# Performance work log

Measured on AMD Instinct MI355X. Metric: run time of the kernel, lower is better.

## Reference

```python
import jax, jax.numpy as jnp
import numpy as np

H, D, DIM = 8, 128, 1024   # heads, dim_head, model dim (inner_dim = H*D = DIM)
QB, N = 16, 512            # 'q' and 'n' dims of the [q, n, dim] inputs


def layer_norm(x, g, b, eps=1e-5):
    mu = x.mean(-1, keepdims=True)
    var = ((x - mu) ** 2).mean(-1, keepdims=True)
    return (x - mu) / jnp.sqrt(var + eps) * g + b


def setup_inputs() -> dict:
    key = jax.random.key(0)
    ks = jax.random.split(key, 8)
    rn = lambda k, shape, s=1.0: jax.random.normal(k, shape, jnp.float32) * s
    return {
        'q': rn(ks[0], (QB, N, DIM)),
        'k': rn(ks[1], (QB, N, DIM)),
        'v': rn(ks[2], (QB, N, DIM)),
        'ln_g': jnp.ones(DIM, jnp.float32),
        'ln_b': jnp.zeros(DIM, jnp.float32),
        'w_in': rn(ks[3], (H * D, DIM), 0.02),          # Linear(dim -> inner_dim), no bias
        'wp_w1': rn(ks[4], (D, 2 * D), 0.05),           # weight_predictor Linear(2d -> d)
        'wp_b1': jnp.zeros(D, jnp.float32),
        'wp_ln_g': jnp.ones(D, jnp.float32),
        'wp_ln_b': jnp.zeros(D, jnp.float32),
        'wp_w2': rn(ks[5], (3, D), 0.05),               # Linear(d -> 3)
        'wp_b2': jnp.zeros(3, jnp.float32),
        'w_out': rn(ks[6], (DIM, H * D), 0.02),         # output Linear(inner_dim -> dim)
        'b_out': jnp.zeros(DIM, jnp.float32),
    }


def reference(q, k, v, ln_g, ln_b, w_in, wp_w1, wp_b1, wp_ln_g, wp_ln_b,
              wp_w2, wp_b2, w_out, b_out):
    def proj(t):
        x = layer_norm(t, ln_g, ln_b) @ w_in.T                 # [Q, N, H*D]
        Qd, Nd = t.shape[0], t.shape[1]
        return x.reshape(Qd, Nd, H, D).transpose(2, 0, 1, 3)   # [h, q, n, d]

    f_q, f_k, f_v = proj(q), proj(k), proj(v)

    # cosine similarity component
    dots = jnp.einsum('hqnd,hqmd->hqnm', f_q, f_k)
    qn = jnp.linalg.norm(f_q, axis=-1)                          # [h, q, n]
    kn = jnp.linalg.norm(f_k, axis=-1)                          # [h, q, m]
    cosine_sim = dots / (qn[..., :, None] * kn[..., None, :])

    q_centered = f_q - f_q.mean(-1, keepdims=True)

    # variance component (unbiased variance, clipped ratio vs target_var=1)
    q_var = jnp.var(f_q, axis=-1, ddof=1)
    k_var = jnp.var(f_k, axis=-1, ddof=1)
    q_ratio = 2.0 * jnp.minimum(q_var, 1.0) / (q_var + 1.0)
    k_ratio = 2.0 * jnp.minimum(k_var, 1.0) / (k_var + 1.0)
    var_component = jnp.einsum('hqn,hqm->hqnm', q_ratio, k_ratio)

    # decorrelation-scaled covariance component (overwrites the dead loop in the source)
    q_flat = q_centered.reshape(H, -1, D)                        # [h, q*n, d]
    feat_corr = jnp.einsum('hnd,hne->hde', q_flat, q_flat) / q_flat.shape[1]
    feat_corr = feat_corr * (1.0 - jnp.eye(D, dtype=feat_corr.dtype))
    decorr_score = jnp.linalg.norm(feat_corr, axis=(-2, -1)) / (D * D)
    decorr_scale = jnp.exp(-5.0 * decorr_score)[:, None, None, None]
    cov_component = cosine_sim * decorr_scale

    # dynamic per-head weight mixing
    q_global = f_q.mean(axis=(1, 2))                             # [h, d]
    k_global = f_k.mean(axis=(1, 2))
    feats = jnp.concatenate([q_global, k_global], axis=-1)       # [h, 2d]
    h1 = jnp.maximum(layer_norm(feats @ wp_w1.T + wp_b1, wp_ln_g, wp_ln_b), 0.0)
    weights = jax.nn.softmax(h1 @ wp_w2.T + wp_b2, axis=-1)      # [h, 3]
    cw = weights[:, 0][:, None, None, None]
    vw = weights[:, 1][:, None, None, None]
    ww = weights[:, 2][:, None, None, None]
    mixed = cw * cosine_sim + vw * cov_component + ww * var_component

    out = jnp.einsum('hqnm,hqmd->hqnd', mixed, f_v)
    out = out.transpose(1, 2, 0, 3).reshape(q.shape[0], q.shape[1], H * D)
    return out @ w_out.T + b_out
```

## Files before the change

### kernel.cpp

```cpp
#include <hip/hip_runtime.h>
#include <hip/hip_bf16.h>

typedef unsigned short u16;
typedef __attribute__((ext_vector_type(8))) short short8;
typedef __attribute__((ext_vector_type(4))) float floatx4;

#define H 8
#define D 128
#define DIM 1024
#define QB 16
#define NSEQ 512
#define R 8192

__device__ inline u16 f2b(float x) {
    union { float f; unsigned int u; } c{x};
    unsigned int lsb = (c.u >> 16) & 1;
    unsigned int r = c.u + 0x7fffu + lsb;
    return (u16)(r >> 16);
}
__device__ inline float b2f(u16 u) {
    union { unsigned int i; float f; } c;
    c.i = (unsigned int)u << 16;
    return c.f;
}

#define GLOAD_LDS16(gptr, lptr)                                                        \
    __builtin_amdgcn_global_load_lds(                                                  \
        (const __attribute__((address_space(1))) unsigned int*)(gptr),                 \
        (__attribute__((address_space(3))) unsigned int*)(lptr), 16, 0, 0)

__global__ __launch_bounds__(256) void ln_all(const float* __restrict__ q,
                                              const float* __restrict__ k,
                                              const float* __restrict__ v,
                                              const float* __restrict__ g,
                                              const float* __restrict__ b,
                                              u16* __restrict__ out) {
    const float* src = (blockIdx.y == 0) ? q : (blockIdx.y == 1) ? k : v;
    int r = blockIdx.x;
    int tid = threadIdx.x;
    const float* row = src + (size_t)r * DIM;
    float4 vv = *(const float4*)(row + tid * 4);
    float sum = vv.x + vv.y + vv.z + vv.w;
    float sq = vv.x * vv.x + vv.y * vv.y + vv.z * vv.z + vv.w * vv.w;
    __shared__ float s1[256], s2[256];
    s1[tid] = sum; s2[tid] = sq;
    __syncthreads();
    for (int s = 128; s > 0; s >>= 1) {
        if (tid < s) { s1[tid] += s1[tid + s]; s2[tid] += s2[tid + s]; }
        __syncthreads();
    }
    float mean = s1[0] * (1.0f / DIM);
    float var = s2[0] * (1.0f / DIM) - mean * mean;
    float rstd = rsqrtf(var + 1e-5f);
    float4 gv = *(const float4*)(g + tid * 4);
    float4 bv = *(const float4*)(b + tid * 4);
    ushort4 pk;
    pk.x = f2b((vv.x - mean) * rstd * gv.x + bv.x);
    pk.y = f2b((vv.y - mean) * rstd * gv.y + bv.y);
    pk.z = f2b((vv.z - mean) * rstd * gv.z + bv.z);
    pk.w = f2b((vv.w - mean) * rstd * gv.w + bv.w);
    *(ushort4*)(out + ((size_t)blockIdx.y * R + r) * DIM + tid * 4) = pk;
}

__global__ __launch_bounds__(256) void cvt2_kernel(const float* __restrict__ a,
                                                   const float* __restrict__ b,
                                                   u16* __restrict__ oa,
                                                   u16* __restrict__ ob, int n4each) {
    int i = blockIdx.x * 256 + threadIdx.x;
    const float* src; u16* dst; int j;
    if (i < n4each) { src = a; dst = oa; j = i; }
    else            { src = b; dst = ob; j = i - n4each; }
    float4 v = *(const float4*)(src + (size_t)j * 4);
    ushort4 pk;
    pk.x = f2b(v.x); pk.y = f2b(v.y); pk.z = f2b(v.z); pk.w = f2b(v.w);
    *(ushort4*)(dst + (size_t)j * 4) = pk;
}

__global__ __launch_bounds__(256) void gemm_qkv(const u16* __restrict__ A,
                                                const u16* __restrict__ B,
                                                u16* __restrict__ qT,
                                                u16* __restrict__ fqb,
                                                u16* __restrict__ kTh,
                                                u16* __restrict__ vT,
                                                float* __restrict__ qn,
                                                float* __restrict__ qm,
                                                float* __restrict__ qr,
                                                float* __restrict__ kn,
                                                float* __restrict__ kr) {
    __shared__ u16 As[128 * 32];
    __shared__ u16 Bs[128 * 32];
    const int tid = threadIdx.x;
    const int m0 = blockIdx.y * 128, n0 = blockIdx.x * 128;
    const int wave = tid >> 6, lane = tid & 63;
    const int wm = (wave >> 1) * 64, wn = (wave & 1) * 64;
    const int fr = lane & 15, kq = lane >> 4;
    const int srow = tid >> 2, scol = (tid & 3) * 8;

    floatx4 acc[4][4] = {};
    const size_t aOff0 = (size_t)(m0 + srow) * DIM + scol;
    const size_t aOff1 = (size_t)(m0 + 64 + srow) * DIM + scol;
    const size_t bOff0 = (size_t)(n0 + srow) * DIM + scol;
    const size_t bOff1 = (size_t)(n0 + 64 + srow) * DIM + scol;

    for (int kt = 0; kt < DIM; kt += 32) {
        GLOAD_LDS16(A + aOff0 + kt, As + tid * 8);
        GLOAD_LDS16(A + aOff1 + kt, As + (256 + tid) * 8);
        GLOAD_LDS16(B + bOff0 + kt, Bs + tid * 8);
        GLOAD_LDS16(B + bOff1 + kt, Bs + (256 + tid) * 8);
        __syncthreads();
        short8 af[4], bf[4];
#pragma unroll
        for (int i = 0; i < 4; i++)
            af[i] = *(const short8*)&As[(wm + i * 16 + fr) * 32 + kq * 8];
#pragma unroll
        for (int j = 0; j < 4; j++)
            bf[j] = *(const short8*)&Bs[(wn + j * 16 + fr) * 32 + kq * 8];
#pragma unroll
        for (int i = 0; i < 4; i++)
#pragma unroll
            for (int j = 0; j < 4; j++)
                acc[i][j] = __builtin_amdgcn_mfma_f32_16x16x32_bf16(af[i], bf[j], acc[i][j], 0, 0, 0);
        __syncthreads();
    }

    const int seg = blockIdx.y >> 6;
    const int lrb = (blockIdx.y & 63) * 128;
    const int h = blockIdx.x;
    float* sred = (float*)As;
    float* invb = (float*)Bs;

    if (seg <= 1) {
        const int half = wn >> 6;
#pragma unroll
        for (int i = 0; i < 4; i++) {
            float s[4] = {}, qs[4] = {};
#pragma unroll
            for (int j = 0; j < 4; j++)
#pragma unroll
                for (int r = 0; r < 4; r++) {
                    float vv = acc[i][j][r];
                    s[r] += vv; qs[r] += vv * vv;
                }
#pragma unroll
            for (int m = 1; m < 16; m <<= 1)
#pragma unroll
                for (int r = 0; r < 4; r++) {
                    s[r] += __shfl_xor(s[r], m);
                    qs[r] += __shfl_xor(qs[r], m);
                }
            if (fr == 0) {
                int row = wm + i * 16 + kq * 4;
#pragma unroll
                for (int r = 0; r < 4; r++) {
                    sred[(row + r) * 4 + half * 2 + 0] = s[r];
                    sred[(row + r) * 4 + half * 2 + 1] = qs[r];
                }
            }
        }
        __syncthreads();
        if (tid < 128) {
            float sum = sred[tid * 4 + 0] + sred[tid * 4 + 2];
            float sq  = sred[tid * 4 + 1] + sred[tid * 4 + 3];
            float nrm = sqrtf(sq);
            float var = (sq - sum * sum * (1.0f / D)) * (1.0f / (D - 1));
            float ratio = 2.0f * fminf(var, 1.0f) / (var + 1.0f);
            size_t idx = (size_t)h * R + lrb + tid;
            if (seg == 0) {
                qn[idx] = nrm; qm[idx] = sum * (1.0f / D); qr[idx] = ratio;
            } else {
                kn[idx] = nrm; kr[idx] = ratio;
                invb[tid] = 1.0f / nrm;
            }
        }
        __syncthreads();
    }

    u16* dstT = (seg == 0) ? qT : (seg == 1) ? kTh : vT;
#pragma unroll
    for (int i = 0; i < 4; i++) {
        const int tr = wm + i * 16 + kq * 4;
        const int lrow = lrb + tr;
        float sc[4] = {1.0f, 1.0f, 1.0f, 1.0f};
        if (seg == 1) {
#pragma unroll
            for (int r = 0; r < 4; r++) sc[r] = invb[tr + r];
        }
#pragma unroll
        for (int j = 0; j < 4; j++) {
            const int cl = wn + j * 16 + fr;
            ushort4 pk;
            pk.x = f2b(acc[i][j][0] * sc[0]);
            pk.y = f2b(acc[i][j][1] * sc[1]);
            pk.z = f2b(acc[i][j][2] * sc[2]);
            pk.w = f2b(acc[i][j][3] * sc[3]);
            *(ushort4*)(dstT + (size_t)(h * D + cl) * R + lrow) = pk;
            if (seg == 0) {
                fqb[(size_t)(lrow + 0) * DIM + h * D + cl] = pk.x;
                fqb[(size_t)(lrow + 1) * DIM + h * D + cl] = pk.y;
                fqb[(size_t)(lrow + 2) * DIM + h * D + cl] = pk.z;
                fqb[(size_t)(lrow + 3) * DIM + h * D + cl] = pk.w;
            }
        }
    }
}

template <int MODE>
__global__ __launch_bounds__(256) void colsum_b(const u16* __restrict__ fT,
                                                const float* __restrict__ wvec,
                                                float* __restrict__ g,
                                                float* __restrict__ u,
                                                float* __restrict__ s2) {
    int dg = blockIdx.x, h = blockIdx.y, tid = threadIdx.x;
    __shared__ float r1[256], r2[256];
    for (int dd = 0; dd < 8; dd++) {
        int d = dg * 8 + dd;
        const u16* rowp = fT + (size_t)(h * D + d) * R;
        float s = 0.0f, su = 0.0f;
        for (int it = 0; it < 32; it++) {
            int r = it * 256 + tid;
            float v = b2f(rowp[r]);
            if (MODE == 2) s += v * wvec[h * R + r];
            else { s += v; su += v * wvec[h * R + r]; }
        }
        r1[tid] = s; r2[tid] = su;
        __syncthreads();
        for (int st = 128; st > 0; st >>= 1) {
            if (tid < st) { r1[tid] += r1[tid + st]; r2[tid] += r2[tid + st]; }
            __syncthreads();
        }
        if (tid == 0) {
            g[h * D + d] = r1[0] * (1.0f / R);
            if (MODE == 1) u[h * D + d] = r2[0];
        }
        __syncthreads();
    }
    if (MODE == 1 && dg == 0) {
        float t = 0.0f;
        for (int it = 0; it < 32; it++) {
            float m = wvec[h * R + it * 256 + tid];
            t += m * m;
        }
        r1[tid] = t;
        __syncthreads();
        for (int st = 128; st > 0; st >>= 1) {
            if (tid < st) r1[tid] += r1[tid + st];
            __syncthreads();
        }
        if (tid == 0) s2[h] = r1[0];
    }
}

__global__ __launch_bounds__(256) void syrk_q(const u16* __restrict__ qT,
                                              float* __restrict__ P) {
    __shared__ u16 As[128 * 32];
    const int c = blockIdx.x, h = blockIdx.y;
    const int tid = threadIdx.x;
    const int wave = tid >> 6, lane = tid & 63;
    const int wm = (wave >> 1) * 64, wn = (wave & 1) * 64;
    const int fr = lane & 15, kq = lane >> 4;
    const int srow = tid >> 2, scol = (tid & 3) * 8;
    floatx4 acc[4][4] = {};
    const size_t a0 = (size_t)(h * D + srow) * R + c * 512 + scol;
    const size_t a1 = (size_t)(h * D + 64 + srow) * R + c * 512 + scol;
    for (int kt = 0; kt < 512; kt += 32) {
        GLOAD_LDS16(qT + a0 + kt, As + tid * 8);
        GLOAD_LDS16(qT + a1 + kt, As + (256 + tid) * 8);
        __syncthreads();
        short8 af[4], bf[4];
#pragma unroll
        for (int i = 0; i < 4; i++)
            af[i] = *(const short8*)&As[(wm + i * 16 + fr) * 32 + kq * 8];
#pragma unroll
        for (int j = 0; j < 4; j++)
            bf[j] = *(const short8*)&As[(wn + j * 16 + fr) * 32 + kq * 8];
#pragma unroll
        for (int i = 0; i < 4; i++)
#pragma unroll
            for (int j = 0; j < 4; j++)
                acc[i][j] = __builtin_amdgcn_mfma_f32_16x16x32_bf16(af[i], bf[j], acc[i][j], 0, 0, 0);
        __syncthreads();
    }
    float* base = P + (size_t)(h * 16 + c) * (D * D);
#pragma unroll
    for (int i = 0; i < 4; i++) {
        int dr = wm + i * 16 + kq * 4;
#pragma unroll
        for (int j = 0; j < 4; j++) {
            int ec = wn + j * 16 + fr;
#pragma unroll
            for (int r = 0; r < 4; r++)
                base[(size_t)(dr + r) * D + ec] = acc[i][j][r];
        }
    }
}

__global__ __launch_bounds__(256) void reduce_fc(const float* __restrict__ P,
                                                 float* __restrict__ fc) {
    int idx = blockIdx.x * 256 + threadIdx.x;
    int h = idx >> 14, de = idx & 16383;
    float s = 0.0f;
    for (int c = 0; c < 16; c++)
        s += P[(size_t)(h * 16 + c) * (D * D) + de];
    fc[idx] = s;
}

__global__ __launch_bounds__(256) void head_kernel(const float* __restrict__ fc,
                                                   const float* __restrict__ ubuf,
                                                   const float* __restrict__ s2b,
                                                   const float* __restrict__ qg,
                                                   const float* __restrict__ kg,
                                                   const float* __restrict__ w1,
                                                   const float* __restrict__ b1,
                                                   const float* __restrict__ lng,
                                                   const float* __restrict__ lnb,
                                                   const float* __restrict__ w2,
                                                   const float* __restrict__ b2,
                                                   float* __restrict__ coef) {
    int h = blockIdx.x, tid = threadIdx.x;
    __shared__ float s1[256], s2[256], s3[256];
    __shared__ float feats[256];
    float s2h = s2b[h];
    float S = 0.0f;
    for (int idx = tid; idx < D * D; idx += 256) {
        int dd = idx >> 7, ee = idx & 127;
        if (dd != ee) {
            float vv = (fc[h * (D * D) + idx] - ubuf[h * D + dd] - ubuf[h * D + ee] + s2h) * (1.0f / R);
            S += vv * vv;
        }
    }
    s1[tid] = S;
    __syncthreads();
    for (int s = 128; s > 0; s >>= 1) {
        if (tid < s) s1[tid] += s1[tid + s];
        __syncthreads();
    }
    float dscale = expf(-5.0f * sqrtf(s1[0]) / (float)(D * D));
    __syncthreads();
    feats[tid] = (tid < 128) ? qg[h * D + tid] : kg[h * D + tid - 128];
    __syncthreads();
    float yv = 0.0f;
    if (tid < 128) {
        float a = b1[tid];
        for (int i = 0; i < 256; i++) a = fmaf(feats[i], w1[tid * 256 + i], a);
        yv = a;
    }
    s1[tid] = (tid < 128) ? yv : 0.0f;
    s2[tid] = (tid < 128) ? yv * yv : 0.0f;
    __syncthreads();
    for (int s = 128; s > 0; s >>= 1) {
        if (tid < s) { s1[tid] += s1[tid + s]; s2[tid] += s2[tid + s]; }
        __syncthreads();
    }
    float mean = s1[0] * (1.0f / 128.0f);
    float var = s2[0] * (1.0f / 128.0f) - mean * mean;
    float rstd = rsqrtf(var + 1e-5f);
    float rel = 0.0f;
    if (tid < 128)
        rel = fmaxf((yv - mean) * rstd * lng[tid] + lnb[tid], 0.0f);
    __syncthreads();
    s1[tid] = (tid < 128) ? rel * w2[0 * 128 + tid] : 0.0f;
    s2[tid] = (tid < 128) ? rel * w2[1 * 128 + tid] : 0.0f;
    s3[tid] = (tid < 128) ? rel * w2[2 * 128 + tid] : 0.0f;
    __syncthreads();
    for (int s = 128; s > 0; s >>= 1) {
        if (tid < s) { s1[tid] += s1[tid + s]; s2[tid] += s2[tid + s]; s3[tid] += s3[tid + s]; }
        __syncthreads();
    }
    if (tid == 0) {
        float g0 = s1[0] + b2[0], g1 = s2[0] + b2[1], g2 = s3[0] + b2[2];
        float mx = fmaxf(g0, fmaxf(g1, g2));
        float e0 = expf(g0 - mx), e1 = expf(g1 - mx), e2 = expf(g2 - mx);
        float inv = 1.0f / (e0 + e1 + e2);
        coef[h * 2 + 0] = e0 * inv + e1 * inv * dscale;
        coef[h * 2 + 1] = e2 * inv;
    }
}

__global__ __launch_bounds__(256) void ktv_mfma(const u16* __restrict__ kTh,
                                                const u16* __restrict__ vT,
                                                const float* __restrict__ kr,
                                                u16* __restrict__ Mt,
                                                float* __restrict__ sv) {
    __shared__ u16 As[128 * 32];
    __shared__ u16 Bs[128 * 32];
    __shared__ float wbuf[32];
    __shared__ float svred[256];
    const int qi = blockIdx.x, h = blockIdx.y;
    const int tid = threadIdx.x;
    const int wave = tid >> 6, lane = tid & 63;
    const int wm = (wave >> 1) * 64, wn = (wave & 1) * 64;
    const int fr = lane & 15, kq = lane >> 4;
    const int srow = tid >> 2, scol = (tid & 3) * 8;
    const int m0g = qi * 512;
    const size_t a0 = (size_t)(h * D + srow) * R + m0g + scol;
    const size_t a1 = (size_t)(h * D + 64 + srow) * R + m0g + scol;
    const int e_id = tid & 127, eh = tid >> 7;
    float svacc = 0.0f;
    floatx4 acc[4][4] = {};
    for (int kt = 0; kt < 512; kt += 32) {
        GLOAD_LDS16(vT + a0 + kt, As + tid * 8);
        GLOAD_LDS16(vT + a1 + kt, As + (256 + tid) * 8);
        GLOAD_LDS16(kTh + a0 + kt, Bs + tid * 8);
        GLOAD_LDS16(kTh + a1 + kt, Bs + (256 + tid) * 8);
        if (tid < 32) wbuf[tid] = kr[(size_t)h * R + m0g + kt + tid];
        __syncthreads();
        short8 af[4], bf[4];
#pragma unroll
        for (int i = 0; i < 4; i++)
            af[i] = *(const short8*)&As[(wm + i * 16 + fr) * 32 + kq * 8];
#pragma unroll
        for (int j = 0; j < 4; j++)
            bf[j] = *(const short8*)&Bs[(wn + j * 16 + fr) * 32 + kq * 8];
#pragma unroll
        for (int i = 0; i < 4; i++)
#pragma unroll
            for (int j = 0; j < 4; j++)
                acc[i][j] = __builtin_amdgcn_mfma_f32_16x16x32_bf16(af[i], bf[j], acc[i][j], 0, 0, 0);
#pragma unroll
        for (int jm = 0; jm < 16; jm++) {
            int mm = eh * 16 + jm;
            svacc += b2f(As[e_id * 32 + mm]) * wbuf[mm];
        }
        __syncthreads();
    }
    u16* mb = Mt + (size_t)(h * QB + qi) * D * D;
#pragma unroll
    for (int i = 0; i < 4; i++) {
        int er = wm + i * 16 + kq * 4;
#pragma unroll
        for (int j = 0; j < 4; j++) {
            int dc = wn + j * 16 + fr;
#pragma unroll
            for (int r = 0; r < 4; r++)
                mb[(size_t)(er + r) * D + dc] = f2b(acc[i][j][r]);
        }
    }
    svred[tid] = svacc;
    __syncthreads();
    if (tid < 128)
        sv[(size_t)(h * QB + qi) * D + tid] = svred[tid] + svred[tid + 128];
}

__global__ __launch_bounds__(256) void attn_mfma(const u16* __restrict__ fqb,
                                                 const u16* __restrict__ Mt,
                                                 const float* __restrict__ qn,
                                                 const float* __restrict__ qr,
                                                 const float* __restrict__ sv,
                                                 const float* __restrict__ coef,
                                                 u16* __restrict__ outb) {
    __shared__ u16 As[128 * 32];
    __shared__ u16 Bs[128 * 32];
    const int nb = blockIdx.x, qi = blockIdx.y, h = blockIdx.z;
    const int tid = threadIdx.x;
    const int wave = tid >> 6, lane = tid & 63;
    const int wm = (wave >> 1) * 64, wn = (wave & 1) * 64;
    const int fr = lane & 15, kq = lane >> 4;
    const int srow = tid >> 2, scol = (tid & 3) * 8;
    const int n0g = qi * 512 + nb * 128;
    const size_t a0 = (size_t)(n0g + srow) * DIM + h * D + scol;
    const size_t a1 = (size_t)(n0g + 64 + srow) * DIM + h * D + scol;
    const u16* mtb = Mt + (size_t)(h * QB + qi) * D * D;
    floatx4 acc[4][4] = {};
    for (int kt = 0; kt < 128; kt += 32) {
        GLOAD_LDS16(fqb + a0 + kt, As + tid * 8);
        GLOAD_LDS16(fqb + a1 + kt, As + (256 + tid) * 8);
        GLOAD_LDS16(mtb + (size_t)srow * D + kt + scol, Bs + tid * 8);
        GLOAD_LDS16(mtb + (size_t)(64 + srow) * D + kt + scol, Bs + (256 + tid) * 8);
        __syncthreads();
        short8 af[4], bf[4];
#pragma unroll
        for (int i = 0; i < 4; i++)
            af[i] = *(const short8*)&As[(wm + i * 16 + fr) * 32 + kq * 8];
#pragma unroll
        for (int j = 0; j < 4; j++)
            bf[j] = *(const short8*)&Bs[(wn + j * 16 + fr) * 32 + kq * 8];
#pragma unroll
        for (int i = 0; i < 4; i++)
#pragma unroll
            for (int j = 0; j < 4; j++)
                acc[i][j] = __builtin_amdgcn_mfma_f32_16x16x32_bf16(af[i], bf[j], acc[i][j], 0, 0, 0);
        __syncthreads();
    }
    float c0 = coef[2 * h], c1 = coef[2 * h + 1];
#pragma unroll
    for (int i = 0; i < 4; i++) {
        int nr = n0g + wm + i * 16 + kq * 4;
        float sc1[4], sc2[4];
#pragma unroll
        for (int r = 0; r < 4; r++) {
            sc1[r] = c0 / qn[(size_t)h * R + nr + r];
            sc2[r] = c1 * qr[(size_t)h * R + nr + r];
        }
#pragma unroll
        for (int j = 0; j < 4; j++) {
            int ec = wn + j * 16 + fr;
            float svv = sv[(size_t)(h * QB + qi) * D + ec];
#pragma unroll
            for (int r = 0; r < 4; r++)
                outb[(size_t)(nr + r) * DIM + h * D + ec] = f2b(sc1[r] * acc[i][j][r] + sc2[r] * svv);
        }
    }
}

__global__ __launch_bounds__(256) void gemm_out(const u16* __restrict__ A,
                                                const u16* __restrict__ B,
                                                const float* __restrict__ bias,
                                                float* __restrict__ C) {
    __shared__ u16 As[128 * 32];
    __shared__ u16 Bs[128 * 32];
    const int tid = threadIdx.x;
    const int m0 = blockIdx.y * 128, n0 = blockIdx.x * 128;
    const int wave = tid >> 6, lane = tid & 63;
    const int wm = (wave >> 1) * 64, wn = (wave & 1) * 64;
    const int fr = lane & 15, kq = lane >> 4;
    const int srow = tid >> 2, scol = (tid & 3) * 8;
    floatx4 acc[4][4] = {};
    const size_t aOff0 = (size_t)(m0 + srow) * DIM + scol;
    const size_t aOff1 = (size_t)(m0 + 64 + srow) * DIM + scol;
    const size_t bOff0 = (size_t)(n0 + srow) * DIM + scol;
    const size_t bOff1 = (size_t)(n0 + 64 + srow) * DIM + scol;
    for (int kt = 0; kt < DIM; kt += 32) {
        GLOAD_LDS16(A + aOff0 + kt, As + tid * 8);
        GLOAD_LDS16(A + aOff1 + kt, As + (256 + tid) * 8);
        GLOAD_LDS16(B + bOff0 + kt, Bs + tid * 8);
        GLOAD_LDS16(B + bOff1 + kt, Bs + (256 + tid) * 8);
        __syncthreads();
        short8 af[4], bf[4];
#pragma unroll
        for (int i = 0; i < 4; i++)
            af[i] = *(const short8*)&As[(wm + i * 16 + fr) * 32 + kq * 8];
#pragma unroll
        for (int j = 0; j < 4; j++)
            bf[j] = *(const short8*)&Bs[(wn + j * 16 + fr) * 32 + kq * 8];
#pragma unroll
        for (int i = 0; i < 4; i++)
#pragma unroll
            for (int j = 0; j < 4; j++)
                acc[i][j] = __builtin_amdgcn_mfma_f32_16x16x32_bf16(af[i], bf[j], acc[i][j], 0, 0, 0);
        __syncthreads();
    }
#pragma unroll
    for (int i = 0; i < 4; i++) {
        int rbase = m0 + wm + i * 16 + kq * 4;
#pragma unroll
        for (int j = 0; j < 4; j++) {
            int col = n0 + wn + j * 16 + fr;
            float badd = bias[col];
#pragma unroll
            for (int r = 0; r < 4; r++)
                C[(size_t)(rbase + r) * DIM + col] = acc[i][j][r] + badd;
        }
    }
}

extern "C" void kernel_launch(void* const* d_in, const int* in_sizes, int n_in,
                              void* d_out, int out_size, void* d_ws, size_t ws_size,
                              hipStream_t stream) {
    (void)in_sizes; (void)n_in; (void)out_size; (void)ws_size;
    const float* q      = (const float*)d_in[0];
    const float* k      = (const float*)d_in[1];
    const float* v      = (const float*)d_in[2];
    const float* ln_g   = (const float*)d_in[3];
    const float* ln_b   = (const float*)d_in[4];
    const float* w_in   = (const float*)d_in[5];
    const float* wp_w1  = (const float*)d_in[6];
    const float* wp_b1  = (const float*)d_in[7];
    const float* wp_lng = (const float*)d_in[8];
    const float* wp_lnb = (const float*)d_in[9];
    const float* wp_w2  = (const float*)d_in[10];
    const float* wp_b2  = (const float*)d_in[11];
    const float* w_out  = (const float*)d_in[12];
    const float* b_out  = (const float*)d_in[13];
    float* out = (float*)d_out;

    constexpr size_t F = (size_t)R * DIM;
    u16* lnall   = (u16*)d_ws;
    u16* fqb     = lnall + 3 * F;
    u16* qT      = fqb + F;
    u16* kTh     = qT + F;
    u16* vT      = kTh + F;
    u16* w_in16  = vT + F;
    u16* w_out16 = w_in16 + (size_t)DIM * DIM;
    u16* Mt      = w_out16 + (size_t)DIM * DIM;
    float* P     = (float*)(Mt + (size_t)H * QB * D * D);
    float* fc    = P + (size_t)16 * H * D * D;
    float* qn    = fc + (size_t)H * D * D;
    float* qm    = qn + (size_t)H * R;
    float* qr    = qm + (size_t)H * R;
    float* kn    = qr + (size_t)H * R;
    float* kr    = kn + (size_t)H * R;
    float* qg    = kr + (size_t)H * R;
    float* kg    = qg + H * D;
    float* ubuf  = kg + H * D;
    float* s2    = ubuf + H * D;
    float* coef  = s2 + H;
    float* svb   = coef + 16;

    cvt2_kernel<<<2048, 256, 0, stream>>>(w_in, w_out, w_in16, w_out16, DIM * DIM / 4);
    ln_all<<<dim3(R, 3), 256, 0, stream>>>(q, k, v, ln_g, ln_b, lnall);

    gemm_qkv<<<dim3(DIM / 128, 3 * R / 128), 256, 0, stream>>>(
        lnall, w_in16, qT, fqb, kTh, vT, qn, qm, qr, kn, kr);

    colsum_b<1><<<dim3(16, H), 256, 0, stream>>>(qT, qm, qg, ubuf, s2);
    colsum_b<2><<<dim3(16, H), 256, 0, stream>>>(kTh, kn, kg, nullptr, nullptr);

    syrk_q<<<dim3(16, H), 256, 0, stream>>>(qT, P);
    reduce_fc<<<512, 256, 0, stream>>>(P, fc);

    head_kernel<<<H, 256, 0, stream>>>(fc, ubuf, s2, qg, kg, wp_w1, wp_b1,
                                       wp_lng, wp_lnb, wp_w2, wp_b2, coef);

    ktv_mfma<<<dim3(QB, H), 256, 0, stream>>>(kTh, vT, kr, Mt, svb);

    attn_mfma<<<dim3(4, QB, H), 256, 0, stream>>>(fqb, Mt, qn, qr, svb, coef, lnall);

    gemm_out<<<dim3(DIM / 128, R / 128), 256, 0, stream>>>(lnall, w_out16, b_out, out);
}
```

Measured before the change: 391.6 us.

## Transpose QKV MFMA operands, coalesce epilogue stores, remap blocks per XCD, fuse reductions

The QKV GEMM swaps MFMA operand order so each lane holds a row's values, which simplifies the row-stat reduction and the transposed stores. The fqb row-major copy is now staged through LDS and written as coalesced vectors. Both GEMMs use a 1D grid remapped so that consecutive row blocks land on the same XCD for L2 reuse. The two colsum launches merge into one, syrk splits K into 32 chunks, and reduce_fc plus the decorrelation sum fold into a parallel decorr_sum kernel in place of the single-block loop. In exchange, the transposed stores are now scalar 16-bit writes, and the larger LDS footprint may lower occupancy.

```diff
diff --git a/kernel.cpp b/kernel.cpp
--- a/kernel.cpp
+++ b/kernel.cpp
@@ -87,10 +87,21 @@
                                                 float* __restrict__ qr,
                                                 float* __restrict__ kn,
                                                 float* __restrict__ kr) {
-    __shared__ u16 As[128 * 32];
-    __shared__ u16 Bs[128 * 32];
+    __shared__ u16 smem[19712];
+    u16* As = smem;
+    u16* Bs = smem + 4096;
+    float* sred = (float*)(smem + 18432);
+    float* invb = (float*)(smem + 19456);
+
     const int tid = threadIdx.x;
-    const int m0 = blockIdx.y * 128, n0 = blockIdx.x * 128;
+    const int bb = blockIdx.x;
+    const int xcd = bb & 7, j0 = bb >> 3;
+    const int h = j0 & 7;
+    const int rowblk = xcd * 24 + (j0 >> 3);
+    const int m0 = rowblk * 128, n0 = h * 128;
+    const int seg = rowblk >> 6;
+    const int lrb = (rowblk & 63) * 128;
+
     const int wave = tid >> 6, lane = tid & 63;
     const int wm = (wave >> 1) * 64, wn = (wave & 1) * 64;
     const int fr = lane & 15, kq = lane >> 4;
@@ -108,53 +119,39 @@
         GLOAD_LDS16(B + bOff0 + kt, Bs + tid * 8);
         GLOAD_LDS16(B + bOff1 + kt, Bs + (256 + tid) * 8);
         __syncthreads();
-        short8 af[4], bf[4];
-#pragma unroll
-        for (int i = 0; i < 4; i++)
-            af[i] = *(const short8*)&As[(wm + i * 16 + fr) * 32 + kq * 8];
+        short8 xf[4], wf[4];
+#pragma unroll
+        for (int i = 0; i < 4; i++)
+            xf[i] = *(const short8*)&As[(wm + i * 16 + fr) * 32 + kq * 8];
 #pragma unroll
         for (int j = 0; j < 4; j++)
-            bf[j] = *(const short8*)&Bs[(wn + j * 16 + fr) * 32 + kq * 8];
-#pragma unroll
-        for (int i = 0; i < 4; i++)
-#pragma unroll
-            for (int j = 0; j < 4; j++)
-                acc[i][j] = __builtin_amdgcn_mfma_f32_16x16x32_bf16(af[i], bf[j], acc[i][j], 0, 0, 0);
-        __syncthreads();
-    }
-
-    const int seg = blockIdx.y >> 6;
-    const int lrb = (blockIdx.y & 63) * 128;
-    const int h = blockIdx.x;
-    float* sred = (float*)As;
-    float* invb = (float*)Bs;
+            wf[j] = *(const short8*)&Bs[(wn + j * 16 + fr) * 32 + kq * 8];
+#pragma unroll
+        for (int j = 0; j < 4; j++)
+#pragma unroll
+            for (int i = 0; i < 4; i++)
+                acc[j][i] = __builtin_amdgcn_mfma_f32_16x16x32_bf16(wf[j], xf[i], acc[j][i], 0, 0, 0);
+        __syncthreads();
+    }
 
     if (seg <= 1) {
         const int half = wn >> 6;
 #pragma unroll
         for (int i = 0; i < 4; i++) {
-            float s[4] = {}, qs[4] = {};
+            float s = 0.0f, qs = 0.0f;
 #pragma unroll
             for (int j = 0; j < 4; j++)
 #pragma unroll
-                for (int r = 0; r < 4; r++) {
-                    float vv = acc[i][j][r];
-                    s[r] += vv; qs[r] += vv * vv;
+                for (int rg = 0; rg < 4; rg++) {
+                    float vv = acc[j][i][rg];
+                    s += vv; qs += vv * vv;
                 }
-#pragma unroll
-            for (int m = 1; m < 16; m <<= 1)
-#pragma unroll
-                for (int r = 0; r < 4; r++) {
-                    s[r] += __shfl_xor(s[r], m);
-                    qs[r] += __shfl_xor(qs[r], m);
-                }
-            if (fr == 0) {
-                int row = wm + i * 16 + kq * 4;
-#pragma unroll
-                for (int r = 0; r < 4; r++) {
-                    sred[(row + r) * 4 + half * 2 + 0] = s[r];
-                    sred[(row + r) * 4 + half * 2 + 1] = qs[r];
-                }
+            s += __shfl_xor(s, 16); qs += __shfl_xor(qs, 16);
+            s += __shfl_xor(s, 32); qs += __shfl_xor(qs, 32);
+            if (kq == 0) {
+                int rl = wm + i * 16 + fr;
+                sred[rl * 4 + half * 2 + 0] = s;
+                sred[rl * 4 + half * 2 + 1] = qs;
             }
         }
         __syncthreads();
@@ -178,39 +175,52 @@
     u16* dstT = (seg == 0) ? qT : (seg == 1) ? kTh : vT;
 #pragma unroll
     for (int i = 0; i < 4; i++) {
-        const int tr = wm + i * 16 + kq * 4;
-        const int lrow = lrb + tr;
-        float sc[4] = {1.0f, 1.0f, 1.0f, 1.0f};
-        if (seg == 1) {
-#pragma unroll
-            for (int r = 0; r < 4; r++) sc[r] = invb[tr + r];
-        }
+        const int rl = wm + i * 16 + fr;
+        const float sc = (seg == 1) ? invb[rl] : 1.0f;
 #pragma unroll
         for (int j = 0; j < 4; j++) {
-            const int cl = wn + j * 16 + fr;
-            ushort4 pk;
-            pk.x = f2b(acc[i][j][0] * sc[0]);
-            pk.y = f2b(acc[i][j][1] * sc[1]);
-            pk.z = f2b(acc[i][j][2] * sc[2]);
-            pk.w = f2b(acc[i][j][3] * sc[3]);
-            *(ushort4*)(dstT + (size_t)(h * D + cl) * R + lrow) = pk;
-            if (seg == 0) {
-                fqb[(size_t)(lrow + 0) * DIM + h * D + cl] = pk.x;
-                fqb[(size_t)(lrow + 1) * DIM + h * D + cl] = pk.y;
-                fqb[(size_t)(lrow + 2) * DIM + h * D + cl] = pk.z;
-                fqb[(size_t)(lrow + 3) * DIM + h * D + cl] = pk.w;
+#pragma unroll
+            for (int rg = 0; rg < 4; rg++) {
+                const int cl = wn + j * 16 + kq * 4 + rg;
+                dstT[(size_t)(h * D + cl) * R + lrb + rl] = f2b(acc[j][i][rg] * sc);
             }
         }
     }
-}
-
-template <int MODE>
-__global__ __launch_bounds__(256) void colsum_b(const u16* __restrict__ fT,
-                                                const float* __restrict__ wvec,
-                                                float* __restrict__ g,
-                                                float* __restrict__ u,
-                                                float* __restrict__ s2) {
-    int dg = blockIdx.x, h = blockIdx.y, tid = threadIdx.x;
+
+    if (seg == 0) {
+        __syncthreads();
+        u16* Tw = smem + wave * 4608;
+#pragma unroll
+        for (int i = 0; i < 4; i++)
+#pragma unroll
+            for (int j = 0; j < 4; j++) {
+                ushort4 pk;
+                pk.x = f2b(acc[j][i][0]); pk.y = f2b(acc[j][i][1]);
+                pk.z = f2b(acc[j][i][2]); pk.w = f2b(acc[j][i][3]);
+                *(ushort4*)&Tw[(i * 16 + fr) * 72 + j * 16 + kq * 4] = pk;
+            }
+        __syncthreads();
+#pragma unroll
+        for (int p = 0; p < 16; p++) {
+            int rloc = p * 4 + kq;
+            int c4 = fr * 4;
+            ushort4 v = *(const ushort4*)&Tw[rloc * 72 + c4];
+            *(ushort4*)&fqb[(size_t)(lrb + wm + rloc) * DIM + h * D + wn + c4] = v;
+        }
+    }
+}
+
+__global__ __launch_bounds__(256) void colsum2(const u16* __restrict__ qT,
+                                               const u16* __restrict__ kTh,
+                                               const float* __restrict__ qm,
+                                               const float* __restrict__ kn,
+                                               float* __restrict__ qg,
+                                               float* __restrict__ kg,
+                                               float* __restrict__ ubuf,
+                                               float* __restrict__ s2) {
+    int dg = blockIdx.x, h = blockIdx.y, mode = blockIdx.z, tid = threadIdx.x;
+    const u16* fT = mode ? kTh : qT;
+    const float* wvec = mode ? kn : qm;
     __shared__ float r1[256], r2[256];
     for (int dd = 0; dd < 8; dd++) {
         int d = dg * 8 + dd;
@@ -219,8 +229,9 @@
         for (int it = 0; it < 32; it++) {
             int r = it * 256 + tid;
             float v = b2f(rowp[r]);
-            if (MODE == 2) s += v * wvec[h * R + r];
-            else { s += v; su += v * wvec[h * R + r]; }
+            float w = wvec[h * R + r];
+            if (mode) s += v * w;
+            else { s += v; su += v * w; }
         }
         r1[tid] = s; r2[tid] = su;
         __syncthreads();
@@ -229,15 +240,15 @@
             __syncthreads();
         }
         if (tid == 0) {
-            g[h * D + d] = r1[0] * (1.0f / R);
-            if (MODE == 1) u[h * D + d] = r2[0];
-        }
-        __syncthreads();
-    }
-    if (MODE == 1 && dg == 0) {
+            if (mode) kg[h * D + d] = r1[0] * (1.0f / R);
+            else { qg[h * D + d] = r1[0] * (1.0f / R); ubuf[h * D + d] = r2[0]; }
+        }
+        __syncthreads();
+    }
+    if (!mode && dg == 0) {
         float t = 0.0f;
         for (int it = 0; it < 32; it++) {
-            float m = wvec[h * R + it * 256 + tid];
+            float m = qm[h * R + it * 256 + tid];
             t += m * m;
         }
         r1[tid] = t;
@@ -260,9 +271,9 @@
     const int fr = lane & 15, kq = lane >> 4;
     const int srow = tid >> 2, scol = (tid & 3) * 8;
     floatx4 acc[4][4] = {};
-    const size_t a0 = (size_t)(h * D + srow) * R + c * 512 + scol;
-    const size_t a1 = (size_t)(h * D + 64 + srow) * R + c * 512 + scol;
-    for (int kt = 0; kt < 512; kt += 32) {
+    const size_t a0 = (size_t)(h * D + srow) * R + c * 256 + scol;
+    const size_t a1 = (size_t)(h * D + 64 + srow) * R + c * 256 + scol;
+    for (int kt = 0; kt < 256; kt += 32) {
         GLOAD_LDS16(qT + a0 + kt, As + tid * 8);
         GLOAD_LDS16(qT + a1 + kt, As + (256 + tid) * 8);
         __syncthreads();
@@ -280,7 +291,7 @@
                 acc[i][j] = __builtin_amdgcn_mfma_f32_16x16x32_bf16(af[i], bf[j], acc[i][j], 0, 0, 0);
         __syncthreads();
     }
-    float* base = P + (size_t)(h * 16 + c) * (D * D);
+    float* base = P + (size_t)(h * 32 + c) * (D * D);
 #pragma unroll
     for (int i = 0; i < 4; i++) {
         int dr = wm + i * 16 + kq * 4;
@@ -294,19 +305,35 @@
     }
 }
 
-__global__ __launch_bounds__(256) void reduce_fc(const float* __restrict__ P,
-                                                 float* __restrict__ fc) {
-    int idx = blockIdx.x * 256 + threadIdx.x;
-    int h = idx >> 14, de = idx & 16383;
-    float s = 0.0f;
-    for (int c = 0; c < 16; c++)
-        s += P[(size_t)(h * 16 + c) * (D * D) + de];
-    fc[idx] = s;
-}
-
-__global__ __launch_bounds__(256) void head_kernel(const float* __restrict__ fc,
-                                                   const float* __restrict__ ubuf,
-                                                   const float* __restrict__ s2b,
+__global__ __launch_bounds__(256) void decorr_sum(const float* __restrict__ P,
+                                                  const float* __restrict__ ubuf,
+                                                  const float* __restrict__ s2b,
+                                                  float* __restrict__ Spart) {
+    int bx = blockIdx.x, h = blockIdx.y, tid = threadIdx.x;
+    float s2h = s2b[h];
+    float S = 0.0f;
+    for (int t = 0; t < 8; t++) {
+        int de = bx * 2048 + t * 256 + tid;
+        int dd = de >> 7, ee = de & 127;
+        float g = 0.0f;
+        for (int c = 0; c < 32; c++)
+            g += P[(size_t)(h * 32 + c) * (D * D) + de];
+        if (dd != ee) {
+            float vv = (g - ubuf[h * D + dd] - ubuf[h * D + ee] + s2h) * (1.0f / R);
+            S += vv * vv;
+        }
+    }
+    __shared__ float r1[256];
+    r1[tid] = S;
+    __syncthreads();
+    for (int st = 128; st > 0; st >>= 1) {
+        if (tid < st) r1[tid] += r1[tid + st];
+        __syncthreads();
+    }
+    if (tid == 0) Spart[h * 8 + bx] = r1[0];
+}
+
+__global__ __launch_bounds__(256) void head_kernel(const float* __restrict__ Spart,
                                                    const float* __restrict__ qg,
                                                    const float* __restrict__ kg,
                                                    const float* __restrict__ w1,
@@ -319,23 +346,9 @@
     int h = blockIdx.x, tid = threadIdx.x;
     __shared__ float s1[256], s2[256], s3[256];
     __shared__ float feats[256];
-    float s2h = s2b[h];
-    float S = 0.0f;
-    for (int idx = tid; idx < D * D; idx += 256) {
-        int dd = idx >> 7, ee = idx & 127;
-        if (dd != ee) {
-            float vv = (fc[h * (D * D) + idx] - ubuf[h * D + dd] - ubuf[h * D + ee] + s2h) * (1.0f / R);
-            S += vv * vv;
-        }
-    }
-    s1[tid] = S;
-    __syncthreads();
-    for (int s = 128; s > 0; s >>= 1) {
-        if (tid < s) s1[tid] += s1[tid + s];
-        __syncthreads();
-    }
-    float dscale = expf(-5.0f * sqrtf(s1[0]) / (float)(D * D));
-    __syncthreads();
+    float Ssum = 0.0f;
+    for (int c = 0; c < 8; c++) Ssum += Spart[h * 8 + c];
+    float dscale = expf(-5.0f * sqrtf(Ssum) / (float)(D * D));
     feats[tid] = (tid < 128) ? qg[h * D + tid] : kg[h * D + tid - 128];
     __syncthreads();
     float yv = 0.0f;
@@ -509,7 +522,10 @@
     __shared__ u16 As[128 * 32];
     __shared__ u16 Bs[128 * 32];
     const int tid = threadIdx.x;
-    const int m0 = blockIdx.y * 128, n0 = blockIdx.x * 128;
+    const int bb = blockIdx.x;
+    const int xcd = bb & 7, jj = bb >> 3;
+    const int col = jj & 7, rowblk = xcd * 8 + (jj >> 3);
+    const int m0 = rowblk * 128, n0 = col * 128;
     const int wave = tid >> 6, lane = tid & 63;
     const int wm = (wave >> 1) * 64, wn = (wave & 1) * 64;
     const int fr = lane & 15, kq = lane >> 4;
@@ -544,11 +560,11 @@
         int rbase = m0 + wm + i * 16 + kq * 4;
 #pragma unroll
         for (int j = 0; j < 4; j++) {
-            int col = n0 + wn + j * 16 + fr;
-            float badd = bias[col];
+            int c = n0 + wn + j * 16 + fr;
+            float badd = bias[c];
 #pragma unroll
             for (int r = 0; r < 4; r++)
-                C[(size_t)(rbase + r) * DIM + col] = acc[i][j][r] + badd;
+                C[(size_t)(rbase + r) * DIM + c] = acc[i][j][r] + badd;
         }
     }
 }
@@ -583,8 +599,7 @@
     u16* w_out16 = w_in16 + (size_t)DIM * DIM;
     u16* Mt      = w_out16 + (size_t)DIM * DIM;
     float* P     = (float*)(Mt + (size_t)H * QB * D * D);
-    float* fc    = P + (size_t)16 * H * D * D;
-    float* qn    = fc + (size_t)H * D * D;
+    float* qn    = P + (size_t)32 * H * D * D;
     float* qm    = qn + (size_t)H * R;
     float* qr    = qm + (size_t)H * R;
     float* kn    = qr + (size_t)H * R;
@@ -593,27 +608,27 @@
     float* kg    = qg + H * D;
     float* ubuf  = kg + H * D;
     float* s2    = ubuf + H * D;
-    float* coef  = s2 + H;
+    float* Spart = s2 + H;
+    float* coef  = Spart + H * 8;
     float* svb   = coef + 16;
 
     cvt2_kernel<<<2048, 256, 0, stream>>>(w_in, w_out, w_in16, w_out16, DIM * DIM / 4);
     ln_all<<<dim3(R, 3), 256, 0, stream>>>(q, k, v, ln_g, ln_b, lnall);
 
-    gemm_qkv<<<dim3(DIM / 128, 3 * R / 128), 256, 0, stream>>>(
-        lnall, w_in16, qT, fqb, kTh, vT, qn, qm, qr, kn, kr);
-
-    colsum_b<1><<<dim3(16, H), 256, 0, stream>>>(qT, qm, qg, ubuf, s2);
-    colsum_b<2><<<dim3(16, H), 256, 0, stream>>>(kTh, kn, kg, nullptr, nullptr);
-
-    syrk_q<<<dim3(16, H), 256, 0, stream>>>(qT, P);
-    reduce_fc<<<512, 256, 0, stream>>>(P, fc);
-
-    head_kernel<<<H, 256, 0, stream>>>(fc, ubuf, s2, qg, kg, wp_w1, wp_b1,
+    gemm_qkv<<<1536, 256, 0, stream>>>(lnall, w_in16, qT, fqb, kTh, vT,
+                                       qn, qm, qr, kn, kr);
+
+    colsum2<<<dim3(16, H, 2), 256, 0, stream>>>(qT, kTh, qm, kn, qg, kg, ubuf, s2);
+
+    syrk_q<<<dim3(32, H), 256, 0, stream>>>(qT, P);
+    decorr_sum<<<dim3(8, H), 256, 0, stream>>>(P, ubuf, s2, Spart);
+
+    head_kernel<<<H, 256, 0, stream>>>(Spart, qg, kg, wp_w1, wp_b1,
                                        wp_lng, wp_lnb, wp_w2, wp_b2, coef);
 
     ktv_mfma<<<dim3(QB, H), 256, 0, stream>>>(kTh, vT, kr, Mt, svb);
 
     attn_mfma<<<dim3(4, QB, H), 256, 0, stream>>>(fqb, Mt, qn, qr, svb, coef, lnall);
 
-    gemm_out<<<dim3(DIM / 128, R / 128), 256, 0, stream>>>(lnall, w_out16, b_out, out);
-}
+    gemm_out<<<512, 256, 0, stream>>>(lnall, w_out16, b_out, out);
+}
```

After: 345.8 us. 1.13x faster.
